# Performance work log

Hardware: AMD Instinct MI355X
Metric: run time of the kernel (lower is better)

Reference implementation:

```python
import jax, jax.numpy as jnp
import numpy as np


def _block_triu_mask(seq_len, rows_per_block, cols_per_block, dtype=jnp.float32):
    # Block upper-triangular mask: block (i, j) is ones iff j >= i.
    tri = jnp.triu(jnp.ones((seq_len, seq_len), dtype=dtype))
    return jnp.kron(tri, jnp.ones((rows_per_block, cols_per_block), dtype=dtype))


def setup_inputs() -> dict:
    key = jax.random.key(0)
    k_x, k_w1, k_w2 = jax.random.split(key, 3)
    seq_len, input_dim, hidden_dim, output_dim = 64, 64, 128, 64
    batch = 256
    x = jax.random.normal(k_x, (batch, seq_len, input_dim), dtype=jnp.float32)
    # kaiming_uniform_(a=sqrt(5)) on [fan_in, fan_out] tensor -> bound = 1/sqrt(fan_in)
    fan1 = seq_len * input_dim
    W1 = jax.random.uniform(k_w1, (seq_len * input_dim, seq_len * hidden_dim),
                            minval=-1.0, maxval=1.0, dtype=jnp.float32) / np.sqrt(fan1)
    b1 = jnp.zeros((seq_len * hidden_dim,), dtype=jnp.float32)
    fan2 = seq_len * hidden_dim
    W2 = jax.random.uniform(k_w2, (seq_len * hidden_dim, seq_len * output_dim),
                            minval=-1.0, maxval=1.0, dtype=jnp.float32) / np.sqrt(fan2)
    b2 = jnp.zeros((seq_len * output_dim,), dtype=jnp.float32)
    return {"x": x, "W1": W1, "b1": b1, "W2": W2, "b2": b2, "seq_len": seq_len}


def reference(x, W1, b1, W2, b2, seq_len):
    batch = x.shape[0]
    input_dim = x.shape[2]
    hidden_dim = W1.shape[1] // seq_len
    output_dim = W2.shape[1] // seq_len
    mask1 = _block_triu_mask(seq_len, input_dim, hidden_dim, W1.dtype)
    mask2 = _block_triu_mask(seq_len, hidden_dim, output_dim, W2.dtype)
    h = x.reshape(batch, seq_len * input_dim)
    h = jnp.matmul(h, W1 * mask1) + b1           # [B, S*H]
    h = jax.nn.relu(h)
    h = jnp.matmul(h, W2 * mask2) + b2           # [B, S*O]
    return h.reshape(batch, seq_len, output_dim)
```

## Files before the change

### kernel.cpp

```cpp
#include <hip/hip_runtime.h>

typedef short bf16x8 __attribute__((ext_vector_type(8)));
typedef float f32x4 __attribute__((ext_vector_type(4)));

__device__ __forceinline__ unsigned short f2bf(float f) {
  unsigned x = __float_as_uint(f);
  return (unsigned short)((x + 0x7fffu + ((x >> 16) & 1u)) >> 16);
}
__device__ __forceinline__ unsigned b32pair(float a, float b) {
  return (unsigned)f2bf(a) | ((unsigned)f2bf(b) << 16);
}

__device__ __forceinline__ int cbase1(int p) {
  const int a = p >> 3, b = p & 7;
  return (a + 1) * (4 * a + b);
}
__device__ __forceinline__ int cbase2(int p) {
  const int a = p >> 1, b = p & 1;
  return (a + 1) * (a + b);
}


__global__ __launch_bounds__(256)
void pack_x(const float* __restrict__ x, unsigned short* __restrict__ img) {
  const int i = (blockIdx.x * 256 + threadIdx.x) * 8;
  const int m = i >> 12, k = i & 4095;
  float q[8];
  *(float4*)(q)     = *(const float4*)(x + i);
  *(float4*)(q + 4) = *(const float4*)(x + i + 4);
  union { unsigned short u[8]; int4 v; } t;
#pragma unroll
  for (int j = 0; j < 8; ++j) t.u[j] = f2bf(q[j]);
  *(int4*)(img + (size_t)m * 4096 + (k ^ ((m & 7) << 3))) = t.v;
}

template<int MODE>
__global__ __launch_bounds__(256, 2)
void gemm_w(const unsigned short* __restrict__ A, const float* __restrict__ W,
            float* __restrict__ P) {
  constexpr int NPAN = (MODE == 1) ? 64 : 32;
  constexpr int AK   = (MODE == 1) ? 4096 : 8192;
  constexpr int N    = (MODE == 1) ? 8192 : 4096;

  __shared__ unsigned short Ws[2][128 * 64];

  const int p  = NPAN - 1 - (int)blockIdx.z;
  const int mt = blockIdx.y;
  const int c  = blockIdx.x;
  const int nt = (MODE == 1) ? (p + 1) : (4 * p + 4);
  const int i0 = c * 8;
  if (i0 >= nt) return;
  const int i1 = (i0 + 8 < nt) ? (i0 + 8) : nt;
  const int bs = (MODE == 1) ? cbase1(p) : cbase2(p);
  float* po = P + ((size_t)(bs + c) * 2 + mt) * 16384;

  const int tid = threadIdx.x, lane = tid & 63, w = tid >> 6;
  const int l15 = lane & 15, quad = lane >> 4;
  const int wm = w >> 1, wn = w & 1;

  const int wr0 = (tid >> 3) * 2;
  const int wc0 = (tid & 7) * 16;
  const float* wsrc = W + (size_t)p * 128 + wc0;
  const int lk = (MODE == 2) ? (2 * p + 1 + (wc0 >> 6)) * 128 : 0x7fffffff;

  int aoff[4][2];
#pragma unroll
  for (int mi = 0; mi < 4; ++mi) {
    const int m = mt * 128 + wm * 64 + mi * 16 + l15;
#pragma unroll
    for (int h = 0; h < 2; ++h)
      aoff[mi][h] = m * AK + ((h * 32 + quad * 8) ^ ((m & 7) << 3));
  }

  float4 wv[8];
  auto loadW = [&](int kt) {
    const float* r0 = wsrc + (size_t)(kt * 64 + wr0) * N;
#pragma unroll
    for (int j = 0; j < 4; ++j) wv[j] = *(const float4*)(r0 + j * 4);
#pragma unroll
    for (int j = 0; j < 4; ++j) wv[4 + j] = *(const float4*)(r0 + N + j * 4);
  };
  auto storeW = [&](int buf, int kt) {
    const float* f = (const float*)wv;
    const int kg = kt * 64 + wr0;
#pragma unroll
    for (int i = 0; i < 16; ++i) {
      const int cc = wc0 + i;
      float v0 = f[i], v1 = f[16 + i];
      if (MODE == 2) { v0 = (kg < lk) ? v0 : 0.f; v1 = (kg + 1 < lk) ? v1 : 0.f; }
      const int sw = ((cc ^ (cc >> 3)) & 7) << 3;
      *(unsigned*)&Ws[buf][cc * 64 + (wr0 ^ sw)] = b32pair(v0, v1);
    }
  };
  auto loadA = [&](bf16x8 (&af)[4][2], int kt) {
    const unsigned short* at = A + (size_t)kt * 64;
#pragma unroll
    for (int mi = 0; mi < 4; ++mi)
#pragma unroll
      for (int h = 0; h < 2; ++h)
        af[mi][h] = *(const bf16x8*)(at + aoff[mi][h]);
  };

  f32x4 acc[4][4];
#pragma unroll
  for (int mi = 0; mi < 4; ++mi)
#pragma unroll
    for (int ni = 0; ni < 4; ++ni)
      acc[mi][ni] = (f32x4){0.f, 0.f, 0.f, 0.f};

  bf16x8 afA[4][2], afB[4][2];

  loadW(i0);
  loadA(afA, i0);
  storeW(0, i0);
  __syncthreads();

  int cur = 0;
  auto ITER = [&](bf16x8 (&caf)[4][2], bf16x8 (&naf)[4][2], int t) {
    const bool pre = (t + 1 < i1);
    if (pre) { loadW(t + 1); loadA(naf, t + 1); }
    const unsigned short* Wb = &Ws[cur][0];
#pragma unroll
    for (int h = 0; h < 2; ++h) {
      const int kk = h * 32;
      bf16x8 bfr[4];
#pragma unroll
      for (int ni = 0; ni < 4; ++ni) {
        const int cc = wn * 64 + ni * 16 + l15;
        const int sw = ((cc ^ (cc >> 3)) & 7) << 3;
        bfr[ni] = *(const bf16x8*)&Wb[cc * 64 + ((kk + quad * 8) ^ sw)];
      }
#pragma unroll
      for (int mi = 0; mi < 4; ++mi)
#pragma unroll
        for (int ni = 0; ni < 4; ++ni)
          acc[mi][ni] = __builtin_amdgcn_mfma_f32_16x16x32_bf16(
              caf[mi][h], bfr[ni], acc[mi][ni], 0, 0, 0);
    }
    if (pre) {
      storeW(cur ^ 1, t + 1);
      __syncthreads();
    }
    cur ^= 1;
  };

  int t = i0;
  while (true) {
    ITER(afA, afB, t); if (++t >= i1) break;
    ITER(afB, afA, t); if (++t >= i1) break;
  }

  float* ps = po + w * 4096 + lane;
#pragma unroll
  for (int mi = 0; mi < 4; ++mi)
#pragma unroll
    for (int ni = 0; ni < 4; ++ni)
#pragma unroll
      for (int r = 0; r < 4; ++r)
        ps[ni * 64 + r * 256 + mi * 1024] = acc[mi][ni][r];
}

__global__ __launch_bounds__(256)
void reduce1(const float* __restrict__ P, const float* __restrict__ b1,
             unsigned short* __restrict__ Hs) {
  const int g = blockIdx.x * 256 + threadIdx.x;
  const int m = g >> 11, n0 = (g & 2047) * 4;
  const int p = n0 >> 7, nl = n0 & 127, mb = m >> 7, ml = m & 127;
  const int s = (((ml >> 2) & 3) * 16 + (nl & 15)) + ((nl >> 4) & 3) * 64
              + (ml & 3) * 256 + ((ml >> 4) & 3) * 1024
              + (((ml >> 6) << 1) + (nl >> 6)) * 4096;
  const int nc = (p + 8) >> 3;
  const float* ps = P + ((size_t)cbase1(p) * 2 + mb) * 16384 + s;
  f32x4 a = *(const f32x4*)ps;
  for (int ci = 1; ci < nc; ++ci)
    a += *(const f32x4*)(ps + (size_t)ci * 32768);
  a += *(const f32x4*)(b1 + n0);
  union { unsigned short u[4]; int2 v; } t;
#pragma unroll
  for (int j = 0; j < 4; ++j) t.u[j] = f2bf(fmaxf(a[j], 0.f));
  *(int2*)(Hs + (size_t)m * 8192 + (n0 ^ ((m & 7) << 3))) = t.v;
}

__global__ __launch_bounds__(256)
void reduce2(const float* __restrict__ P, const float* __restrict__ b2,
             float* __restrict__ out) {
  const int g = blockIdx.x * 256 + threadIdx.x;
  const int m = g >> 10, n0 = (g & 1023) * 4;
  const int p = n0 >> 7, nl = n0 & 127, mb = m >> 7, ml = m & 127;
  const int s = (((ml >> 2) & 3) * 16 + (nl & 15)) + ((nl >> 4) & 3) * 64
              + (ml & 3) * 256 + ((ml >> 4) & 3) * 1024
              + (((ml >> 6) << 1) + (nl >> 6)) * 4096;
  const int nc = (p + 2) >> 1;
  const float* ps = P + ((size_t)cbase2(p) * 2 + mb) * 16384 + s;
  f32x4 a = *(const f32x4*)ps;
  for (int ci = 1; ci < nc; ++ci)
    a += *(const f32x4*)(ps + (size_t)ci * 32768);
  a += *(const f32x4*)(b2 + n0);
  *(f32x4*)(out + (size_t)m * 4096 + n0) = a;
}

extern "C" void kernel_launch(void* const* d_in, const int* in_sizes, int n_in,
                              void* d_out, int out_size, void* d_ws, size_t ws_size,
                              hipStream_t stream) {
  const float* x  = (const float*)d_in[0];
  const float* W1 = (const float*)d_in[1];
  const float* b1 = (const float*)d_in[2];
  const float* W2 = (const float*)d_in[3];
  const float* b2 = (const float*)d_in[4];

  char* ws = (char*)d_ws;
  unsigned short* Ximg = (unsigned short*)ws;
  unsigned short* Hs   = (unsigned short*)(ws + 2097152);
  float*          P    = (float*)(ws + 6291456);
  float* out = (float*)d_out;

  pack_x<<<dim3(512), 256, 0, stream>>>(x, Ximg);

  gemm_w<1><<<dim3(8, 2, 64), 256, 0, stream>>>(Ximg, W1, P);

  reduce1<<<dim3(2048), 256, 0, stream>>>(P, b1, Hs);

  gemm_w<2><<<dim3(16, 2, 32), 256, 0, stream>>>(Hs, W2, P);

  reduce2<<<dim3(1024), 256, 0, stream>>>(P, b2, out);
}
```

Measured before the change: 354.7 us.

## Retile masked GEMMs to full-M by 64-column panels, aligning panels to mask blocks

Changes the GEMM tiling from 128x128 tiles split over two M-tiles to 256-row by 64-column panels. Each block covers the whole batch, and each W element is loaded once instead of once per M-tile. For the second GEMM, 64-wide panels line up with the block-triangular mask, so the per-element masking in the W store is dropped and only the needed K tiles are iterated. Panel base offsets, split-K counts and the partial-sum layout are recomputed, with matching changes in the reduce kernels. The trade-off is more, smaller-N blocks, each holding a 256x64 accumulator, and changed split-K partial counts.

```diff
diff --git a/kernel.cpp b/kernel.cpp
--- a/kernel.cpp
+++ b/kernel.cpp
@@ -12,12 +12,13 @@
 }
 
 __device__ __forceinline__ int cbase1(int p) {
-  const int a = p >> 3, b = p & 7;
-  return (a + 1) * (4 * a + b);
+  const int a = p >> 1, b = p & 1;
+  const int u = a >> 3, v = a & 7;
+  return 2 * (4 * u * (u - 1) + v * u + a) + b * ((a + 8) >> 3);
 }
 __device__ __forceinline__ int cbase2(int p) {
-  const int a = p >> 1, b = p & 1;
-  return (a + 1) * (a + b);
+  const int w = p >> 2, r = p & 3;
+  return 2 * w * (w - 1) + r * w + p;
 }
 
 
@@ -38,58 +39,52 @@
 __global__ __launch_bounds__(256, 2)
 void gemm_w(const unsigned short* __restrict__ A, const float* __restrict__ W,
             float* __restrict__ P) {
-  constexpr int NPAN = (MODE == 1) ? 64 : 32;
+  constexpr int NPAN = (MODE == 1) ? 128 : 64;
   constexpr int AK   = (MODE == 1) ? 4096 : 8192;
   constexpr int N    = (MODE == 1) ? 8192 : 4096;
 
-  __shared__ unsigned short Ws[2][128 * 64];
-
-  const int p  = NPAN - 1 - (int)blockIdx.z;
-  const int mt = blockIdx.y;
-  const int c  = blockIdx.x;
-  const int nt = (MODE == 1) ? (p + 1) : (4 * p + 4);
+  __shared__ unsigned short Ws[2][64 * 64];
+
+  const int p = NPAN - 1 - (int)blockIdx.z;
+  const int c = blockIdx.x;
+  const int nt = (MODE == 1) ? ((p >> 1) + 1) : (2 * p + 2);
   const int i0 = c * 8;
   if (i0 >= nt) return;
   const int i1 = (i0 + 8 < nt) ? (i0 + 8) : nt;
   const int bs = (MODE == 1) ? cbase1(p) : cbase2(p);
-  float* po = P + ((size_t)(bs + c) * 2 + mt) * 16384;
+  float* po = P + (size_t)(bs + c) * 16384;
 
   const int tid = threadIdx.x, lane = tid & 63, w = tid >> 6;
   const int l15 = lane & 15, quad = lane >> 4;
-  const int wm = w >> 1, wn = w & 1;
 
   const int wr0 = (tid >> 3) * 2;
-  const int wc0 = (tid & 7) * 16;
-  const float* wsrc = W + (size_t)p * 128 + wc0;
-  const int lk = (MODE == 2) ? (2 * p + 1 + (wc0 >> 6)) * 128 : 0x7fffffff;
+  const int wc0 = (tid & 7) * 8;
+  const float* wsrc = W + (size_t)p * 64 + wc0;
 
   int aoff[4][2];
 #pragma unroll
   for (int mi = 0; mi < 4; ++mi) {
-    const int m = mt * 128 + wm * 64 + mi * 16 + l15;
+    const int m = w * 64 + mi * 16 + l15;
 #pragma unroll
     for (int h = 0; h < 2; ++h)
       aoff[mi][h] = m * AK + ((h * 32 + quad * 8) ^ ((m & 7) << 3));
   }
 
-  float4 wv[8];
+  float4 wv[4];
   auto loadW = [&](int kt) {
     const float* r0 = wsrc + (size_t)(kt * 64 + wr0) * N;
-#pragma unroll
-    for (int j = 0; j < 4; ++j) wv[j] = *(const float4*)(r0 + j * 4);
-#pragma unroll
-    for (int j = 0; j < 4; ++j) wv[4 + j] = *(const float4*)(r0 + N + j * 4);
-  };
-  auto storeW = [&](int buf, int kt) {
+    wv[0] = *(const float4*)(r0);
+    wv[1] = *(const float4*)(r0 + 4);
+    wv[2] = *(const float4*)(r0 + N);
+    wv[3] = *(const float4*)(r0 + N + 4);
+  };
+  auto storeW = [&](int buf) {
     const float* f = (const float*)wv;
-    const int kg = kt * 64 + wr0;
-#pragma unroll
-    for (int i = 0; i < 16; ++i) {
+#pragma unroll
+    for (int i = 0; i < 8; ++i) {
       const int cc = wc0 + i;
-      float v0 = f[i], v1 = f[16 + i];
-      if (MODE == 2) { v0 = (kg < lk) ? v0 : 0.f; v1 = (kg + 1 < lk) ? v1 : 0.f; }
       const int sw = ((cc ^ (cc >> 3)) & 7) << 3;
-      *(unsigned*)&Ws[buf][cc * 64 + (wr0 ^ sw)] = b32pair(v0, v1);
+      *(unsigned*)&Ws[buf][cc * 64 + (wr0 ^ sw)] = b32pair(f[i], f[8 + i]);
     }
   };
   auto loadA = [&](bf16x8 (&af)[4][2], int kt) {
@@ -112,21 +107,20 @@
 
   loadW(i0);
   loadA(afA, i0);
-  storeW(0, i0);
+  storeW(0);
   __syncthreads();
 
-  int cur = 0;
-  auto ITER = [&](bf16x8 (&caf)[4][2], bf16x8 (&naf)[4][2], int t) {
+  auto ITER = [&](bf16x8 (&caf)[4][2], bf16x8 (&naf)[4][2], int t, int buf) {
     const bool pre = (t + 1 < i1);
     if (pre) { loadW(t + 1); loadA(naf, t + 1); }
-    const unsigned short* Wb = &Ws[cur][0];
+    const unsigned short* Wb = &Ws[buf][0];
 #pragma unroll
     for (int h = 0; h < 2; ++h) {
       const int kk = h * 32;
       bf16x8 bfr[4];
 #pragma unroll
       for (int ni = 0; ni < 4; ++ni) {
-        const int cc = wn * 64 + ni * 16 + l15;
+        const int cc = ni * 16 + l15;
         const int sw = ((cc ^ (cc >> 3)) & 7) << 3;
         bfr[ni] = *(const bf16x8*)&Wb[cc * 64 + ((kk + quad * 8) ^ sw)];
       }
@@ -138,16 +132,14 @@
               caf[mi][h], bfr[ni], acc[mi][ni], 0, 0, 0);
     }
     if (pre) {
-      storeW(cur ^ 1, t + 1);
+      storeW(buf ^ 1);
       __syncthreads();
     }
-    cur ^= 1;
-  };
-
-  int t = i0;
-  while (true) {
-    ITER(afA, afB, t); if (++t >= i1) break;
-    ITER(afB, afA, t); if (++t >= i1) break;
+  };
+
+  for (int t = i0; t < i1; t += 2) {
+    ITER(afA, afB, t, 0);
+    if (t + 1 < i1) ITER(afB, afA, t + 1, 1);
   }
 
   float* ps = po + w * 4096 + lane;
@@ -165,15 +157,14 @@
              unsigned short* __restrict__ Hs) {
   const int g = blockIdx.x * 256 + threadIdx.x;
   const int m = g >> 11, n0 = (g & 2047) * 4;
-  const int p = n0 >> 7, nl = n0 & 127, mb = m >> 7, ml = m & 127;
-  const int s = (((ml >> 2) & 3) * 16 + (nl & 15)) + ((nl >> 4) & 3) * 64
-              + (ml & 3) * 256 + ((ml >> 4) & 3) * 1024
-              + (((ml >> 6) << 1) + (nl >> 6)) * 4096;
-  const int nc = (p + 8) >> 3;
-  const float* ps = P + ((size_t)cbase1(p) * 2 + mb) * 16384 + s;
+  const int p = n0 >> 6, nl = n0 & 63;
+  const int s = ((m >> 2) & 3) * 16 + (nl & 15) + (nl >> 4) * 64
+              + (m & 3) * 256 + ((m >> 4) & 3) * 1024 + (m >> 6) * 4096;
+  const int nc = ((p >> 1) + 8) >> 3;
+  const float* ps = P + (size_t)cbase1(p) * 16384 + s;
   f32x4 a = *(const f32x4*)ps;
   for (int ci = 1; ci < nc; ++ci)
-    a += *(const f32x4*)(ps + (size_t)ci * 32768);
+    a += *(const f32x4*)(ps + (size_t)ci * 16384);
   a += *(const f32x4*)(b1 + n0);
   union { unsigned short u[4]; int2 v; } t;
 #pragma unroll
@@ -186,15 +177,14 @@
              float* __restrict__ out) {
   const int g = blockIdx.x * 256 + threadIdx.x;
   const int m = g >> 10, n0 = (g & 1023) * 4;
-  const int p = n0 >> 7, nl = n0 & 127, mb = m >> 7, ml = m & 127;
-  const int s = (((ml >> 2) & 3) * 16 + (nl & 15)) + ((nl >> 4) & 3) * 64
-              + (ml & 3) * 256 + ((ml >> 4) & 3) * 1024
-              + (((ml >> 6) << 1) + (nl >> 6)) * 4096;
-  const int nc = (p + 2) >> 1;
-  const float* ps = P + ((size_t)cbase2(p) * 2 + mb) * 16384 + s;
+  const int p = n0 >> 6, nl = n0 & 63;
+  const int s = ((m >> 2) & 3) * 16 + (nl & 15) + (nl >> 4) * 64
+              + (m & 3) * 256 + ((m >> 4) & 3) * 1024 + (m >> 6) * 4096;
+  const int nc = (p >> 2) + 1;
+  const float* ps = P + (size_t)cbase2(p) * 16384 + s;
   f32x4 a = *(const f32x4*)ps;
   for (int ci = 1; ci < nc; ++ci)
-    a += *(const f32x4*)(ps + (size_t)ci * 32768);
+    a += *(const f32x4*)(ps + (size_t)ci * 16384);
   a += *(const f32x4*)(b2 + n0);
   *(f32x4*)(out + (size_t)m * 4096 + n0) = a;
 }
@@ -216,11 +206,11 @@
 
   pack_x<<<dim3(512), 256, 0, stream>>>(x, Ximg);
 
-  gemm_w<1><<<dim3(8, 2, 64), 256, 0, stream>>>(Ximg, W1, P);
+  gemm_w<1><<<dim3(8, 1, 128), 256, 0, stream>>>(Ximg, W1, P);
 
   reduce1<<<dim3(2048), 256, 0, stream>>>(P, b1, Hs);
 
-  gemm_w<2><<<dim3(16, 2, 32), 256, 0, stream>>>(Hs, W2, P);
+  gemm_w<2><<<dim3(16, 1, 64), 256, 0, stream>>>(Hs, W2, P);
 
   reduce2<<<dim3(1024), 256, 0, stream>>>(P, b2, out);
 }
```

After: 332.4 us. 6.3% less time.
